# Performance work log

Hardware: AMD Instinct MI355X
Metric: run time of the kernel (lower is better)

## Reference

```python
import jax, jax.numpy as jnp
import numpy as np

KH = KW = 3
PAD = 1
STRIDE = 1
C_IN = 32
C_OUT = 16
H = W = 64
B = 64
H_OUT = (H - KH + 2 * PAD) // STRIDE + 1
W_OUT = (W - KW + 2 * PAD) // STRIDE + 1
S = H_OUT * W_OUT
K = C_IN * KH * KW


def unfold_2d(x):
    # x: [B, C, H, W] -> [B, C*KH*KW, S], torch.nn.functional.unfold ordering
    xp = jnp.pad(x, ((0, 0), (0, 0), (PAD, PAD), (PAD, PAD)))
    patches = []
    for i in range(KH):
        for j in range(KW):
            patches.append(xp[:, :, i:i + H_OUT * STRIDE:STRIDE, j:j + W_OUT * STRIDE:STRIDE])
    u = jnp.stack(patches, axis=2)  # [B, C, KH*KW, H_OUT, W_OUT]
    return u.reshape(x.shape[0], K, S)


def setup_inputs() -> dict:
    key = jax.random.key(0)
    k1, k2, k3 = jax.random.split(key, 3)
    X = jax.random.normal(k1, (B, C_IN, H, W), dtype=jnp.float32)
    # kaiming normal (linear): std = 1/sqrt(fan_in), fan_in = K for each location's GEMM
    weight = jax.random.normal(k2, (S, K, C_OUT), dtype=jnp.float32) / jnp.sqrt(jnp.float32(K))
    # xavier uniform over [H_OUT, W_OUT]
    lim = np.sqrt(6.0 / (H_OUT + W_OUT))
    bias = jax.random.uniform(k3, (H_OUT, W_OUT), dtype=jnp.float32, minval=-lim, maxval=lim)
    return {"X": X, "weight": weight, "bias": bias}


def reference(X, weight, bias):
    ufld = unfold_2d(X)                               # [B, K, S]
    ufld = ufld + bias.reshape(1, 1, -1)              # bias added per-location to patches
    h = jnp.einsum('bks,skc->bcs', ufld, weight)      # per-location unshared GEMM
    return h.reshape(X.shape[0], C_OUT, H_OUT, W_OUT)
```

## Files before the change

kernel.cpp:

```cpp
#include <hip/hip_runtime.h>
#include <stdint.h>
#include <stddef.h>

#define HOUT 64
#define WOUT 64
#define CIN  32
#define COUT 16
#define SLOC 4096
#define KTOT 288
#define HPAD 66
#define WPAD 148

typedef __attribute__((ext_vector_type(8))) short  short8;
typedef __attribute__((ext_vector_type(4))) float  floatx4;

static __device__ __forceinline__ unsigned short f2bf(float f) {
    union { float f; unsigned int u; } v; v.f = f;
    unsigned int u = v.u;
    unsigned int r = (u + 0x7FFFu + ((u >> 16) & 1u)) >> 16;
    return (unsigned short)r;
}

__global__ __launch_bounds__(256) void prep_kernel(const float* __restrict__ X,
                                                   unsigned short* __restrict__ xt) {
    const int id  = blockIdx.x;
    const int tid = threadIdx.x;

    if (id < 260) {
        int h1, w1;
        if (id < 66)       { h1 = 0;  w1 = id; }
        else if (id < 132) { h1 = 65; w1 = id - 66; }
        else { int r = id - 132; h1 = (r >> 1) + 1; w1 = (r & 1) ? 65 : 0; }
        ((uint4*)(xt + (size_t)(h1 * HPAD + w1) * 2048))[tid] = uint4{0u, 0u, 0u, 0u};
    }

    const int w   = tid >> 2;
    const int cg8 = (tid & 3) * 8;
#pragma unroll
    for (int u = 0; u < 2; ++u) {
        const int unit = id * 2 + u;
        const int h = unit >> 6, b = unit & 63;
        const float* xb = X + (((size_t)b * CIN + cg8) * HOUT + h) * WOUT + w;
        unsigned short v[8];
#pragma unroll
        for (int j = 0; j < 8; ++j)
            v[j] = f2bf(xb[(size_t)j * HOUT * WOUT]);
        uint4 pack;
        pack.x = (unsigned)v[0] | ((unsigned)v[1] << 16);
        pack.y = (unsigned)v[2] | ((unsigned)v[3] << 16);
        pack.z = (unsigned)v[4] | ((unsigned)v[5] << 16);
        pack.w = (unsigned)v[6] | ((unsigned)v[7] << 16);
        *(uint4*)(xt + (size_t)((h + 1) * HPAD + (w + 1)) * 2048 + b * CIN + cg8) = pack;
    }
}

__global__ __launch_bounds__(512, 4) void varconv_kernel(const unsigned short* __restrict__ xt,
                                                         const float* __restrict__ Wg,
                                                         const float* __restrict__ bias,
                                                         float* __restrict__ out) {
    __shared__ __align__(16) unsigned int wru[2][2][16 * WPAD];
    __shared__ float cs[2][2][4][16];

    const int id   = blockIdx.x;
    const int s0   = id * 8;
    const int y    = s0 >> 6;
    const int x0   = s0 & 63;
    const int tid  = threadIdx.x;
    const int lane = tid & 63;
    const int wv   = tid >> 6;
    const int q4   = wv & 3;
    const int sh   = wv >> 2;
    const int gtid = q4 * 64 + lane;
    const int q    = lane >> 4;
    const int n    = lane & 15;
    const int B0   = q4 * 16;

    floatx4 acc[4];
#pragma unroll
    for (int i = 0; i < 4; ++i) acc[i] = floatx4{0.f, 0.f, 0.f, 0.f};

    auto stage = [&](int P, int BUF) {
        const int S = s0 + 4 * sh + P;
        const uint4* wsrc = (const uint4*)(Wg + (size_t)S * (KTOT * COUT));
        unsigned int* wb = &wru[BUF][sh][0];
        float cacc[4] = {0.f, 0.f, 0.f, 0.f};
#pragma unroll
        for (int it = 0; it < 3; ++it) {
            const int tau = gtid + it * 256;
            if (tau < 576) {
                const int ng = tau & 3;
                const int cp = (tau >> 2) & 15;
                const int t  = tau >> 6;
                const int kA = 18 * cp + t;
                union { uint4 u; float f[4]; } fA, fB;
                fA.u = wsrc[kA * 4 + ng];
                fB.u = wsrc[(kA + 9) * 4 + ng];
#pragma unroll
                for (int m = 0; m < 4; ++m) {
                    cacc[m] += fA.f[m] + fB.f[m];
                    wb[(4 * ng + m) * WPAD + t * 16 + cp] =
                        (unsigned)f2bf(fA.f[m]) | ((unsigned)f2bf(fB.f[m]) << 16);
                }
            }
        }
#pragma unroll
        for (int m = 0; m < 4; ++m) {
            cacc[m] += __shfl_xor(cacc[m], 4, 64);
            cacc[m] += __shfl_xor(cacc[m], 8, 64);
            cacc[m] += __shfl_xor(cacc[m], 16, 64);
            cacc[m] += __shfl_xor(cacc[m], 32, 64);
        }
        if (lane < 4) {
#pragma unroll
            for (int m = 0; m < 4; ++m)
                cs[BUF][sh][q4][4 * lane + m] = cacc[m];
        }
    };

    auto compute = [&](int P, int BUF, floatx4& a) {
        const int sl = 4 * sh + P;
        const int S  = s0 + sl;
        const int x  = x0 + sl;
        short8 af[9], bf[9];
#pragma unroll
        for (int t = 0; t < 9; ++t) {
            const int cy = t / 3, cx = t % 3;
            af[t] = *(const short8*)(xt + (size_t)((y + cy) * HPAD + (x + cx)) * 2048
                                        + (B0 + n) * CIN + q * 8);
        }
#pragma unroll
        for (int t = 0; t < 9; ++t)
            bf[t] = *(const short8*)&wru[BUF][sh][n * WPAD + t * 16 + 4 * q];
        const float badd = bias[S] * (cs[BUF][sh][0][n] + cs[BUF][sh][1][n]
                                    + cs[BUF][sh][2][n] + cs[BUF][sh][3][n]);
#pragma unroll
        for (int t = 0; t < 9; ++t)
            a = __builtin_amdgcn_mfma_f32_16x16x32_bf16(af[t], bf[t], a, 0, 0, 0);
        a[0] += badd; a[1] += badd; a[2] += badd; a[3] += badd;
    };

    stage(0, 0);
    __syncthreads();
#pragma unroll
    for (int p = 0; p < 4; ++p) {
        const int buf = p & 1;
        if (p < 3) stage(p + 1, buf ^ 1);
        compute(p, buf, acc[p]);
        __syncthreads();
    }

#pragma unroll
    for (int r = 0; r < 4; ++r) {
        const int b = B0 + 4 * q + r;
        float* dst = out + ((size_t)(b * COUT + n)) * SLOC + s0 + 4 * sh;
        *(floatx4*)dst = floatx4{acc[0][r], acc[1][r], acc[2][r], acc[3][r]};
    }
}

extern "C" void kernel_launch(void* const* d_in, const int* in_sizes, int n_in,
                              void* d_out, int out_size, void* d_ws, size_t ws_size,
                              hipStream_t stream) {
    const float* X    = (const float*)d_in[0];
    const float* Wg   = (const float*)d_in[1];
    const float* bias = (const float*)d_in[2];
    float* out = (float*)d_out;

    unsigned short* xt = (unsigned short*)d_ws;

    prep_kernel<<<2048, 256, 0, stream>>>(X, xt);
    varconv_kernel<<<512, 512, 0, stream>>>(xt, Wg, bias, out);
}
```

Measured before the change: 165.4 us.

## Split varconv into smaller 2-location blocks with single-shot weight staging

Restructures the main kernel from 512 blocks of 512 threads handling 8 locations with a double-buffered staging pipeline into 2048 blocks of 256 threads handling 2 adjacent locations each. Both locations' weights are staged to LDS up front with one barrier, and block IDs are swizzled so concurrently running blocks spread across the spatial grid. This aims to raise occupancy and parallelism and remove per-step barriers, at the cost of losing overlap between weight staging and MFMA compute, using narrower 8-byte output stores, and sharing each weight tile across fewer batch rows.

```diff
diff --git a/kernel.cpp b/kernel.cpp
--- a/kernel.cpp
+++ b/kernel.cpp
@@ -13,6 +13,7 @@
 
 typedef __attribute__((ext_vector_type(8))) short  short8;
 typedef __attribute__((ext_vector_type(4))) float  floatx4;
+typedef __attribute__((ext_vector_type(2))) float  floatx2;
 
 static __device__ __forceinline__ unsigned short f2bf(float f) {
     union { float f; unsigned int u; } v; v.f = f;
@@ -54,106 +55,113 @@
     }
 }
 
-__global__ __launch_bounds__(512, 4) void varconv_kernel(const unsigned short* __restrict__ xt,
+__global__ __launch_bounds__(256, 8) void varconv_kernel(const unsigned short* __restrict__ xt,
                                                          const float* __restrict__ Wg,
                                                          const float* __restrict__ bias,
                                                          float* __restrict__ out) {
-    __shared__ __align__(16) unsigned int wru[2][2][16 * WPAD];
-    __shared__ float cs[2][2][4][16];
+    __shared__ __align__(16) unsigned int wru[2][16 * WPAD];
+    __shared__ float cs[2][4][16];
 
     const int id   = blockIdx.x;
-    const int s0   = id * 8;
+    const int sg   = (id & 7) * 256 + (id >> 3);
+    const int s0   = sg * 2;
     const int y    = s0 >> 6;
     const int x0   = s0 & 63;
     const int tid  = threadIdx.x;
     const int lane = tid & 63;
     const int wv   = tid >> 6;
-    const int q4   = wv & 3;
-    const int sh   = wv >> 2;
-    const int gtid = q4 * 64 + lane;
     const int q    = lane >> 4;
     const int n    = lane & 15;
-    const int B0   = q4 * 16;
+    const int B0   = wv * 16;
 
-    floatx4 acc[4];
+    const uint4* wsrc = (const uint4*)(Wg + (size_t)s0 * (KTOT * COUT));
+    float cacc0[4] = {0.f, 0.f, 0.f, 0.f};
+    float cacc1[4] = {0.f, 0.f, 0.f, 0.f};
+
+#define STTASK(T2, SITE, CACC)                                                 \
+    {                                                                          \
+        const int ng = (T2) & 3, cp = ((T2) >> 2) & 15, t = (T2) >> 6;         \
+        const int kA = 18 * cp + t;                                            \
+        union { uint4 u; float f[4]; } fA, fB;                                 \
+        fA.u = wsrc[(SITE) * 1152 + kA * 4 + ng];                              \
+        fB.u = wsrc[(SITE) * 1152 + (kA + 9) * 4 + ng];                        \
+        unsigned int* wb = &wru[SITE][0];                                      \
+        _Pragma("unroll")                                                      \
+        for (int m = 0; m < 4; ++m) {                                          \
+            CACC[m] += fA.f[m] + fB.f[m];                                      \
+            wb[(4 * ng + m) * WPAD + t * 16 + cp] =                            \
+                (unsigned)f2bf(fA.f[m]) | ((unsigned)f2bf(fB.f[m]) << 16);     \
+        }                                                                      \
+    }
+
 #pragma unroll
-    for (int i = 0; i < 4; ++i) acc[i] = floatx4{0.f, 0.f, 0.f, 0.f};
+    for (int it = 0; it < 5; ++it) {
+        const int tau = tid + it * 256;
+        if (tau < 576) {
+            STTASK(tau, 0, cacc0)
+        } else if (tau < 1152) {
+            const int t2 = tau - 576;
+            STTASK(t2, 1, cacc1)
+        }
+    }
+#undef STTASK
 
-    auto stage = [&](int P, int BUF) {
-        const int S = s0 + 4 * sh + P;
-        const uint4* wsrc = (const uint4*)(Wg + (size_t)S * (KTOT * COUT));
-        unsigned int* wb = &wru[BUF][sh][0];
-        float cacc[4] = {0.f, 0.f, 0.f, 0.f};
 #pragma unroll
-        for (int it = 0; it < 3; ++it) {
-            const int tau = gtid + it * 256;
-            if (tau < 576) {
-                const int ng = tau & 3;
-                const int cp = (tau >> 2) & 15;
-                const int t  = tau >> 6;
-                const int kA = 18 * cp + t;
-                union { uint4 u; float f[4]; } fA, fB;
-                fA.u = wsrc[kA * 4 + ng];
-                fB.u = wsrc[(kA + 9) * 4 + ng];
-#pragma unroll
-                for (int m = 0; m < 4; ++m) {
-                    cacc[m] += fA.f[m] + fB.f[m];
-                    wb[(4 * ng + m) * WPAD + t * 16 + cp] =
-                        (unsigned)f2bf(fA.f[m]) | ((unsigned)f2bf(fB.f[m]) << 16);
-                }
-            }
-        }
+    for (int m = 0; m < 4; ++m) {
+        cacc0[m] += __shfl_xor(cacc0[m], 4, 64);
+        cacc1[m] += __shfl_xor(cacc1[m], 4, 64);
+        cacc0[m] += __shfl_xor(cacc0[m], 8, 64);
+        cacc1[m] += __shfl_xor(cacc1[m], 8, 64);
+        cacc0[m] += __shfl_xor(cacc0[m], 16, 64);
+        cacc1[m] += __shfl_xor(cacc1[m], 16, 64);
+        cacc0[m] += __shfl_xor(cacc0[m], 32, 64);
+        cacc1[m] += __shfl_xor(cacc1[m], 32, 64);
+    }
+    if (lane < 4) {
 #pragma unroll
         for (int m = 0; m < 4; ++m) {
-            cacc[m] += __shfl_xor(cacc[m], 4, 64);
-            cacc[m] += __shfl_xor(cacc[m], 8, 64);
-            cacc[m] += __shfl_xor(cacc[m], 16, 64);
-            cacc[m] += __shfl_xor(cacc[m], 32, 64);
+            cs[0][wv][4 * lane + m] = cacc0[m];
+            cs[1][wv][4 * lane + m] = cacc1[m];
         }
-        if (lane < 4) {
+    }
+
+    __syncthreads();
+
+    floatx4 acc[2];
 #pragma unroll
-            for (int m = 0; m < 4; ++m)
-                cs[BUF][sh][q4][4 * lane + m] = cacc[m];
-        }
-    };
+    for (int i = 0; i < 2; ++i) acc[i] = floatx4{0.f, 0.f, 0.f, 0.f};
 
-    auto compute = [&](int P, int BUF, floatx4& a) {
-        const int sl = 4 * sh + P;
-        const int S  = s0 + sl;
-        const int x  = x0 + sl;
-        short8 af[9], bf[9];
-#pragma unroll
-        for (int t = 0; t < 9; ++t) {
-            const int cy = t / 3, cx = t % 3;
-            af[t] = *(const short8*)(xt + (size_t)((y + cy) * HPAD + (x + cx)) * 2048
-                                        + (B0 + n) * CIN + q * 8);
-        }
-#pragma unroll
-        for (int t = 0; t < 9; ++t)
-            bf[t] = *(const short8*)&wru[BUF][sh][n * WPAD + t * 16 + 4 * q];
-        const float badd = bias[S] * (cs[BUF][sh][0][n] + cs[BUF][sh][1][n]
-                                    + cs[BUF][sh][2][n] + cs[BUF][sh][3][n]);
-#pragma unroll
-        for (int t = 0; t < 9; ++t)
-            a = __builtin_amdgcn_mfma_f32_16x16x32_bf16(af[t], bf[t], a, 0, 0, 0);
-        a[0] += badd; a[1] += badd; a[2] += badd; a[3] += badd;
-    };
+#define COMPUTE(I)                                                             \
+    {                                                                          \
+        const int x = x0 + (I);                                                \
+        short8 af[9], bf[9];                                                   \
+        _Pragma("unroll")                                                      \
+        for (int t = 0; t < 9; ++t) {                                          \
+            const int cy = t / 3, cx = t % 3;                                  \
+            af[t] = *(const short8*)(xt + (size_t)((y + cy) * HPAD + (x + cx)) * 2048 \
+                                        + (B0 + n) * CIN + q * 8);             \
+        }                                                                      \
+        _Pragma("unroll")                                                      \
+        for (int t = 0; t < 9; ++t)                                            \
+            bf[t] = *(const short8*)&wru[I][n * WPAD + t * 16 + 4 * q];        \
+        const float badd = bias[s0 + (I)] * (cs[I][0][n] + cs[I][1][n]        \
+                                           + cs[I][2][n] + cs[I][3][n]);       \
+        _Pragma("unroll")                                                      \
+        for (int t = 0; t < 9; ++t)                                            \
+            acc[I] = __builtin_amdgcn_mfma_f32_16x16x32_bf16(af[t], bf[t], acc[I], 0, 0, 0); \
+        acc[I][0] += badd; acc[I][1] += badd;                                  \
+        acc[I][2] += badd; acc[I][3] += badd;                                  \
+    }
 
-    stage(0, 0);
-    __syncthreads();
-#pragma unroll
-    for (int p = 0; p < 4; ++p) {
-        const int buf = p & 1;
-        if (p < 3) stage(p + 1, buf ^ 1);
-        compute(p, buf, acc[p]);
-        __syncthreads();
-    }
+    COMPUTE(0)
+    COMPUTE(1)
+#undef COMPUTE
 
 #pragma unroll
     for (int r = 0; r < 4; ++r) {
         const int b = B0 + 4 * q + r;
-        float* dst = out + ((size_t)(b * COUT + n)) * SLOC + s0 + 4 * sh;
-        *(floatx4*)dst = floatx4{acc[0][r], acc[1][r], acc[2][r], acc[3][r]};
+        float* dst = out + ((size_t)(b * COUT + n)) * SLOC + s0;
+        *(floatx2*)dst = floatx2{acc[0][r], acc[1][r]};
     }
 }
 
@@ -168,5 +176,5 @@
     unsigned short* xt = (unsigned short*)d_ws;
 
     prep_kernel<<<2048, 256, 0, stream>>>(X, xt);
-    varconv_kernel<<<512, 512, 0, stream>>>(xt, Wg, bias, out);
+    varconv_kernel<<<2048, 256, 0, stream>>>(xt, Wg, bias, out);
 }
```

Measured after the change: 163.3 us. Within noise of the previous version (-1.3%).
